# Kernel optimization log

Measured on AMD Instinct MI355X. Metric: run time of the kernel, lower is better.

Reference implementation:

```python
import jax, jax.numpy as jnp
import numpy as np

GROUPS = 8
EPS = 1e-5


def group_norm(x, gamma, beta):
    b, c, h, w = x.shape
    xg = x.reshape(b, GROUPS, c // GROUPS, h, w)
    mu = jnp.mean(xg, axis=(2, 3, 4), keepdims=True)
    var = jnp.mean((xg - mu) ** 2, axis=(2, 3, 4), keepdims=True)
    xn = ((xg - mu) * jax.lax.rsqrt(var + EPS)).reshape(b, c, h, w)
    return xn * gamma[None, :, None, None] + beta[None, :, None, None]


def setup_inputs() -> dict:
    key = jax.random.key(0)
    ks = jax.random.split(key, 4)
    b, c, h, w = 4, 64, 64, 64
    x = jax.random.normal(ks[0], (b, c, h, w), dtype=jnp.float32)
    gamma = jnp.ones((c,), dtype=jnp.float32)
    beta = jnp.zeros((c,), dtype=jnp.float32)
    w_qkv = jax.random.normal(ks[1], (3 * c, c), dtype=jnp.float32) * (1.0 / np.sqrt(c))
    b_qkv = jnp.zeros((3 * c,), dtype=jnp.float32)
    w_proj = jax.random.normal(ks[2], (c, c), dtype=jnp.float32) * (1.0 / np.sqrt(c))
    b_proj = jnp.zeros((c,), dtype=jnp.float32)
    return {"x": x, "gamma": gamma, "beta": beta, "w_qkv": w_qkv,
            "b_qkv": b_qkv, "w_proj": w_proj, "b_proj": b_proj}


def reference(x, gamma, beta, w_qkv, b_qkv, w_proj, b_proj):
    b, c, h, w = x.shape
    xn = group_norm(x, gamma, beta)
    # 1x1 conv == per-pixel linear: [b,3c,h,w]
    qkv = jnp.einsum('oc,bchw->bohw', w_qkv, xn) + b_qkv[None, :, None, None]
    q, k, v = jnp.split(qkv, 3, axis=1)
    # flatten spatial -> tokens: [b, hw, c]
    def tok(t):
        return t.reshape(b, c, h * w).transpose(0, 2, 1)
    q, k, v = tok(q), tok(k), tok(v)
    scale = c ** (-0.5)
    attn = jnp.einsum('bqc,bkc->bqk', q, k) * scale  # [b, hw, hw]
    attn = jax.nn.softmax(attn, axis=-1)
    out = jnp.einsum('bqk,bkc->bqc', attn, v)  # [b, hw, c]
    out = out.transpose(0, 2, 1).reshape(b, c, h, w)
    out = jnp.einsum('oc,bchw->bohw', w_proj, out) + b_proj[None, :, None, None]
    return out + x
```

## Files before the change

kernel.cpp:

```cpp
#include <hip/hip_runtime.h>

typedef __bf16 bf16x8 __attribute__((ext_vector_type(8)));
typedef __bf16 bf16x4 __attribute__((ext_vector_type(4)));
typedef float  f32x4  __attribute__((ext_vector_type(4)));
typedef float  f32x16 __attribute__((ext_vector_type(16)));

#define GLD_LDS16(gsrc, ldst) \
  __builtin_amdgcn_global_load_lds((const __attribute__((address_space(1))) void*)(gsrc), \
                                   (__attribute__((address_space(3))) void*)(ldst), 16, 0, 0)

__device__ inline unsigned cvt_pk_bf16(float lo, float hi) {
  unsigned r;
  asm("v_cvt_pk_bf16_f32 %0, %1, %2" : "=v"(r) : "v"(lo), "v"(hi));
  return r;
}
__device__ inline void pl32_swap(unsigned& a, unsigned& b) {
  asm volatile("v_permlane32_swap_b32 %0, %1" : "+v"(a), "+v"(b));
}
__device__ inline f32x16 zero16() {
  f32x16 z;
#pragma unroll
  for (int i = 0; i < 16; ++i) z[i] = 0.f;
  return z;
}

__global__ __launch_bounds__(256) void gn_partial_k(const float* __restrict__ x,
                                                    const float* __restrict__ w_qkv,
                                                    float* __restrict__ partial,
                                                    __bf16* __restrict__ whi,
                                                    __bf16* __restrict__ wlo) {
  __shared__ float red[2][4];
  const int t = threadIdx.x;
  if (blockIdx.x < 48) {
    const int idx = blockIdx.x * 256 + t;
    float wv = w_qkv[idx];
    __bf16 hh = (__bf16)wv;
    whi[idx] = hh;
    wlo[idx] = (__bf16)(wv - (float)hh);
  }
  const float4* base = (const float4*)(x + (size_t)blockIdx.x * 4096);
  float s = 0.f, sq = 0.f;
#pragma unroll
  for (int kk = 0; kk < 4; ++kk) {
    float4 v = base[t + kk * 256];
    s  += (v.x + v.y) + (v.z + v.w);
    sq += (v.x * v.x + v.y * v.y) + (v.z * v.z + v.w * v.w);
  }
#pragma unroll
  for (int o = 32; o >= 1; o >>= 1) {
    s  += __shfl_down(s, o, 64);
    sq += __shfl_down(sq, o, 64);
  }
  if ((t & 63) == 0) { red[0][t >> 6] = s; red[1][t >> 6] = sq; }
  __syncthreads();
  if (t == 0) {
    float S  = (red[0][0] + red[0][1]) + (red[0][2] + red[0][3]);
    float SQ = (red[1][0] + red[1][1]) + (red[1][2] + red[1][3]);
    partial[blockIdx.x * 2]     = S;
    partial[blockIdx.x * 2 + 1] = SQ;
  }
}

__global__ void gn_final_k(const float* __restrict__ partial,
                           const float* __restrict__ gamma,
                           const float* __restrict__ beta,
                           float* __restrict__ sc) {
  const int t = threadIdx.x;
  __shared__ float mu_s[32], rs_s[32];
  if (t < 32) {
    float S = 0.f, SQ = 0.f;
#pragma unroll
    for (int i = 0; i < 8; ++i) {
      S  += partial[(t * 8 + i) * 2];
      SQ += partial[(t * 8 + i) * 2 + 1];
    }
    float mean = S * (1.f / 32768.f);
    float var  = SQ * (1.f / 32768.f) - mean * mean;
    mu_s[t] = mean;
    rs_s[t] = rsqrtf(fmaxf(var, 0.f) + 1e-5f);
  }
  __syncthreads();
  const int b = t >> 6, c = t & 63;
  const int g = b * 8 + (c >> 3);
  float scale = rs_s[g] * gamma[c];
  sc[t * 2]     = scale;
  sc[t * 2 + 1] = beta[c] - mu_s[g] * scale;
}

__global__ __launch_bounds__(256) void qkv_k(const float* __restrict__ x,
                                             const float* __restrict__ sc,
                                             const __bf16* __restrict__ whi,
                                             const __bf16* __restrict__ wlo,
                                             const float* __restrict__ b_qkv,
                                             __bf16* __restrict__ qo,
                                             __bf16* __restrict__ ko,
                                             __bf16* __restrict__ vto) {
  const int tid  = threadIdx.x;
  const int lane = tid & 63, w = tid >> 6;
  const int px16 = lane & 15, grp = lane >> 4;
  const int b    = blockIdx.x >> 6;
  const int s0   = (blockIdx.x & 63) * 64;
  const int pxg  = s0 + w * 16 + px16;

  bf16x8 bh[2], bl[2];
#pragma unroll
  for (int kk = 0; kk < 2; ++kk) {
    bf16x8 hv, lv;
#pragma unroll
    for (int i = 0; i < 8; ++i) {
      const int c = kk * 32 + grp * 8 + i;
      float xv = x[((size_t)(b * 64 + c) * 4096) + pxg];
      float2 s = *(const float2*)(sc + (b * 64 + c) * 2);
      float xn = fmaf(xv, s.x, s.y);
      __bf16 hh = (__bf16)xn;
      hv[i] = hh;
      lv[i] = (__bf16)(xn - (float)hh);
    }
    bh[kk] = hv;
    bl[kk] = lv;
  }

  f32x4 acc[12];
#pragma unroll
  for (int ot = 0; ot < 12; ++ot) {
    const int o = ot * 16 + px16;
    f32x4 a = {0.f, 0.f, 0.f, 0.f};
#pragma unroll
    for (int kk = 0; kk < 2; ++kk) {
      const size_t wo = (size_t)o * 64 + kk * 32 + grp * 8;
      bf16x8 ah = *(const bf16x8*)(whi + wo);
      bf16x8 al = *(const bf16x8*)(wlo + wo);
      a = __builtin_amdgcn_mfma_f32_16x16x32_bf16(ah, bh[kk], a, 0, 0, 0);
      a = __builtin_amdgcn_mfma_f32_16x16x32_bf16(ah, bl[kk], a, 0, 0, 0);
      a = __builtin_amdgcn_mfma_f32_16x16x32_bf16(al, bh[kk], a, 0, 0, 0);
    }
    acc[ot] = a;
  }

#pragma unroll
  for (int ot = 0; ot < 4; ++ot) {
    const int ob = ot * 16 + grp * 4;
    float4 bias = *(const float4*)(b_qkv + ob);
    f32x4 a = acc[ot];
    bf16x4 qv = {(__bf16)((a[0] + bias.x) * 0.18033688f),
                 (__bf16)((a[1] + bias.y) * 0.18033688f),
                 (__bf16)((a[2] + bias.z) * 0.18033688f),
                 (__bf16)((a[3] + bias.w) * 0.18033688f)};
    *(bf16x4*)(qo + ((size_t)b * 4096 + pxg) * 64 + ob) = qv;
  }
#pragma unroll
  for (int ot = 4; ot < 8; ++ot) {
    const int ob = (ot - 4) * 16 + grp * 4;
    float4 bias = *(const float4*)(b_qkv + 64 + ob);
    f32x4 a = acc[ot];
    bf16x4 kv = {(__bf16)(a[0] + bias.x), (__bf16)(a[1] + bias.y),
                 (__bf16)(a[2] + bias.z), (__bf16)(a[3] + bias.w)};
    *(bf16x4*)(ko + ((size_t)b * 4096 + pxg) * 64 + ob) = kv;
  }
#pragma unroll
  for (int ot = 8; ot < 12; ++ot) {
    const int ob = (ot - 8) * 16 + grp * 4;
    float4 bias = *(const float4*)(b_qkv + 128 + ob);
    f32x4 a = acc[ot];
#pragma unroll
    for (int r = 0; r < 4; ++r) {
      float bv = (r == 0) ? bias.x : (r == 1) ? bias.y : (r == 2) ? bias.z : bias.w;
      vto[((size_t)(b * 64 + ob + r)) * 4096 + pxg] = (__bf16)(a[r] + bv);
    }
  }
}

__global__ __launch_bounds__(512, 2) void attn_k(const __bf16* __restrict__ q,
                                                 const __bf16* __restrict__ k,
                                                 const __bf16* __restrict__ vt,
                                                 __bf16* __restrict__ opart,
                                                 float* __restrict__ mlpart) {
  __shared__ __bf16 k_lds[3][4096];
  __shared__ __bf16 v_lds[3][4096];

  const int tid  = threadIdx.x;
  const int lane = tid & 63, w = tid >> 6;
  const int col  = lane & 31;
  const int h    = lane >> 5;
  const int swz  = col & 7;

  const int blk  = blockIdx.x;
  const int xcd  = blk & 7;
  const int b    = xcd >> 1;
  const int rest = blk >> 3;
  const int seg  = rest >> 3;
  const int qblk = (rest & 7) | ((xcd & 1) << 3);
  const int q0   = qblk * 256 + w * 32;
  const int j0b  = seg * 512;

  const __bf16* qp = q  + (size_t)b * 4096 * 64;
  const __bf16* kp = k  + (size_t)b * 4096 * 64;
  const __bf16* vp = vt + (size_t)b * 64 * 4096;

  bf16x8 qf[4];
#pragma unroll
  for (int kk = 0; kk < 4; ++kk)
    qf[kk] = *(const bf16x8*)(qp + (size_t)(q0 + col) * 64 + kk * 16 + h * 8);
  __builtin_amdgcn_sched_barrier(0);

  f32x16 acc0 = zero16(), acc1 = zero16();
  float m = -1e30f, l = 0.f;

  const int soff = tid * 16;
  const int sj = soff >> 7;
  const int sc2 = ((soff >> 4) & 7) ^ (sj & 7);

  auto stage = [&](int buf, int j0) {
    GLD_LDS16(kp + (size_t)(j0 + sj) * 64 + sc2 * 8, (char*)(&k_lds[buf][0]) + soff);
    GLD_LDS16(vp + (size_t)sj * 4096 + j0 + sc2 * 8, (char*)(&v_lds[buf][0]) + soff);
  };

  stage(0, j0b);
  stage(1, j0b + 64);

#pragma unroll
  for (int kt = 0; kt < 8; ++kt) {
    if (kt < 7) asm volatile("s_waitcnt vmcnt(2)" ::: "memory");
    else        asm volatile("s_waitcnt vmcnt(0)" ::: "memory");
    __builtin_amdgcn_s_barrier();

    if (kt < 6) stage((kt + 2) % 3, j0b + (kt + 2) * 64);

    const char* kbase = (const char*)&k_lds[kt % 3][0];
    const char* vbase = (const char*)&v_lds[kt % 3][0];

    f32x16 sa0 = zero16(), sa1 = zero16();
    __builtin_amdgcn_s_setprio(1);
#pragma unroll
    for (int kk = 0; kk < 4; ++kk) {
      bf16x8 kf0 = *(const bf16x8*)(kbase + col * 128        + (((2 * kk + h) ^ swz) << 4));
      bf16x8 kf1 = *(const bf16x8*)(kbase + (32 + col) * 128 + (((2 * kk + h) ^ swz) << 4));
      sa0 = __builtin_amdgcn_mfma_f32_32x32x16_bf16(kf0, qf[kk], sa0, 0, 0, 0);
      sa1 = __builtin_amdgcn_mfma_f32_32x32x16_bf16(kf1, qf[kk], sa1, 0, 0, 0);
    }
    __builtin_amdgcn_s_setprio(0);

    float x0 = fmaxf(fmaxf(sa0[0], sa0[1]),   fmaxf(sa0[2], sa0[3]));
    float x1 = fmaxf(fmaxf(sa0[4], sa0[5]),   fmaxf(sa0[6], sa0[7]));
    float x2 = fmaxf(fmaxf(sa0[8], sa0[9]),   fmaxf(sa0[10], sa0[11]));
    float x3 = fmaxf(fmaxf(sa0[12], sa0[13]), fmaxf(sa0[14], sa0[15]));
    float y0 = fmaxf(fmaxf(sa1[0], sa1[1]),   fmaxf(sa1[2], sa1[3]));
    float y1 = fmaxf(fmaxf(sa1[4], sa1[5]),   fmaxf(sa1[6], sa1[7]));
    float y2 = fmaxf(fmaxf(sa1[8], sa1[9]),   fmaxf(sa1[10], sa1[11]));
    float y3 = fmaxf(fmaxf(sa1[12], sa1[13]), fmaxf(sa1[14], sa1[15]));
    float mx = fmaxf(fmaxf(fmaxf(x0, x1), fmaxf(x2, x3)),
                     fmaxf(fmaxf(y0, y1), fmaxf(y2, y3)));
    mx = fmaxf(mx, __shfl_xor(mx, 32, 64));
    float mn = fmaxf(m, mx);
    float sf = exp2f(m - mn);
    m = mn;
    float ls = 0.f;
#pragma unroll
    for (int r = 0; r < 16; ++r) { sa0[r] = exp2f(sa0[r] - mn); ls += sa0[r]; }
#pragma unroll
    for (int r = 0; r < 16; ++r) { sa1[r] = exp2f(sa1[r] - mn); ls += sa1[r]; }
    l = l * sf + ls;
    acc0 *= sf;
    acc1 *= sf;

    unsigned w0[8], w1[8];
#pragma unroll
    for (int qd = 0; qd < 4; ++qd) {
      w0[qd * 2]     = cvt_pk_bf16(sa0[4 * qd],     sa0[4 * qd + 1]);
      w0[qd * 2 + 1] = cvt_pk_bf16(sa0[4 * qd + 2], sa0[4 * qd + 3]);
      w1[qd * 2]     = cvt_pk_bf16(sa1[4 * qd],     sa1[4 * qd + 1]);
      w1[qd * 2 + 1] = cvt_pk_bf16(sa1[4 * qd + 2], sa1[4 * qd + 3]);
    }
    bf16x8 pa[4];
#pragma unroll
    for (int c = 0; c < 4; ++c) {
      const unsigned* wt = (c < 2) ? w0 : w1;
      unsigned a0 = wt[(2 * (c & 1)) * 2],     b0 = wt[(2 * (c & 1) + 1) * 2];
      unsigned a1 = wt[(2 * (c & 1)) * 2 + 1], b1 = wt[(2 * (c & 1) + 1) * 2 + 1];
      pl32_swap(a0, b0);
      pl32_swap(a1, b1);
      uint4 u; u.x = a0; u.y = a1; u.z = b0; u.w = b1;
      pa[c] = __builtin_bit_cast(bf16x8, u);
    }

    __builtin_amdgcn_s_setprio(1);
#pragma unroll
    for (int c = 0; c < 4; ++c) {
      bf16x8 vf0 = *(const bf16x8*)(vbase + col * 128        + (((2 * c + h) ^ swz) << 4));
      bf16x8 vf1 = *(const bf16x8*)(vbase + (32 + col) * 128 + (((2 * c + h) ^ swz) << 4));
      acc0 = __builtin_amdgcn_mfma_f32_32x32x16_bf16(vf0, pa[c], acc0, 0, 0, 0);
      acc1 = __builtin_amdgcn_mfma_f32_32x32x16_bf16(vf1, pa[c], acc1, 0, 0, 0);
    }
    __builtin_amdgcn_s_setprio(0);
  }

  float lf = l + __shfl_xor(l, 32, 64);
  const int qrow = q0 + col;
  __bf16* ob = opart + ((size_t)(b * 8 + seg) * 4096 + qrow) * 64;
#pragma unroll
  for (int rq = 0; rq < 4; ++rq) {
    const int d0 = 8 * rq + 4 * h;
    bf16x4 o0 = {(__bf16)acc0[4 * rq], (__bf16)acc0[4 * rq + 1],
                 (__bf16)acc0[4 * rq + 2], (__bf16)acc0[4 * rq + 3]};
    bf16x4 o1 = {(__bf16)acc1[4 * rq], (__bf16)acc1[4 * rq + 1],
                 (__bf16)acc1[4 * rq + 2], (__bf16)acc1[4 * rq + 3]};
    *(bf16x4*)(ob + d0)      = o0;
    *(bf16x4*)(ob + 32 + d0) = o1;
  }
  if (h == 0) {
    float2 mlv; mlv.x = m; mlv.y = lf;
    *(float2*)(mlpart + ((size_t)(b * 8 + seg) * 4096 + qrow) * 2) = mlv;
  }
}

__global__ __launch_bounds__(256) void proj_k(const __bf16* __restrict__ opart,
                                              const float* __restrict__ mlpart,
                                              const float* __restrict__ x,
                                              const float* __restrict__ w_proj,
                                              const float* __restrict__ b_proj,
                                              float* __restrict__ out) {
  __shared__ float wseg[8][32];
  __shared__ float a_lds[32 * 68];
  __shared__ float o_lds[64 * 33];
  const int t  = threadIdx.x;
  const int b  = blockIdx.x >> 7;
  const int s0 = (blockIdx.x & 127) * 32;

  if (t < 32) {
    const int rowg = s0 + t;
    float ms[8], ls[8], es[8];
    float M = -1e30f;
#pragma unroll
    for (int s = 0; s < 8; ++s) {
      float2 ml = *(const float2*)(mlpart + ((size_t)(b * 8 + s) * 4096 + rowg) * 2);
      ms[s] = ml.x; ls[s] = ml.y;
      M = fmaxf(M, ms[s]);
    }
    float L = 0.f;
#pragma unroll
    for (int s = 0; s < 8; ++s) { es[s] = exp2f(ms[s] - M); L += es[s] * ls[s]; }
    float invL = 1.f / L;
#pragma unroll
    for (int s = 0; s < 8; ++s) wseg[s][t] = es[s] * invL;
  }
  __syncthreads();

  for (int i = t; i < 512; i += 256) {
    const int px = i >> 4, c4 = i & 15;
    const __bf16* obase = opart + ((size_t)(b * 8) * 4096 + s0 + px) * 64 + c4 * 4;
    float4 a = {0.f, 0.f, 0.f, 0.f};
#pragma unroll
    for (int s = 0; s < 8; ++s) {
      bf16x4 v = *(const bf16x4*)(obase + (size_t)s * 4096 * 64);
      float wv = wseg[s][px];
      a.x += wv * (float)v[0]; a.y += wv * (float)v[1];
      a.z += wv * (float)v[2]; a.w += wv * (float)v[3];
    }
    *(float4*)(&a_lds[px * 68 + c4 * 4]) = a;
  }

  const int o = t & 63, wg = t >> 6;
  float4 wr[16];
  const float4* wrow = (const float4*)(w_proj + o * 64);
#pragma unroll
  for (int i = 0; i < 16; ++i) wr[i] = wrow[i];
  const float bias = b_proj[o];
  __syncthreads();

  for (int pp = 0; pp < 8; ++pp) {
    const int px = wg * 8 + pp;
    const float4* ar = (const float4*)&a_lds[px * 68];
    float a0 = bias, a1 = 0.f, a2 = 0.f, a3 = 0.f;
#pragma unroll
    for (int i = 0; i < 16; i += 4) {
      float4 x0 = ar[i], x1 = ar[i + 1], x2 = ar[i + 2], x3 = ar[i + 3];
      a0 += wr[i    ].x * x0.x + wr[i    ].y * x0.y + wr[i    ].z * x0.z + wr[i    ].w * x0.w;
      a1 += wr[i + 1].x * x1.x + wr[i + 1].y * x1.y + wr[i + 1].z * x1.z + wr[i + 1].w * x1.w;
      a2 += wr[i + 2].x * x2.x + wr[i + 2].y * x2.y + wr[i + 2].z * x2.z + wr[i + 2].w * x2.w;
      a3 += wr[i + 3].x * x3.x + wr[i + 3].y * x3.y + wr[i + 3].z * x3.z + wr[i + 3].w * x3.w;
    }
    o_lds[o * 33 + px] = (a0 + a1) + (a2 + a3);
  }
  __syncthreads();
  for (int idx = t; idx < 2048; idx += 256) {
    const int c = idx >> 5, px = idx & 31;
    const size_t gi = ((size_t)(b * 64 + c)) * 4096 + s0 + px;
    out[gi] = o_lds[c * 33 + px] + x[gi];
  }
}

extern "C" void kernel_launch(void* const* d_in, const int* in_sizes, int n_in,
                              void* d_out, int out_size, void* d_ws, size_t ws_size,
                              hipStream_t stream) {
  const float* x      = (const float*)d_in[0];
  const float* gamma  = (const float*)d_in[1];
  const float* beta   = (const float*)d_in[2];
  const float* w_qkv  = (const float*)d_in[3];
  const float* b_qkv  = (const float*)d_in[4];
  const float* w_proj = (const float*)d_in[5];
  const float* b_proj = (const float*)d_in[6];
  float* out = (float*)d_out;

  char* ws = (char*)d_ws;
  float*  partial = (float*)ws;
  float*  scbuf   = partial + 512;
  __bf16* whi     = (__bf16*)(ws + 4096);
  __bf16* wlo     = whi + 12288;
  __bf16* qb  = (__bf16*)(ws + 65536);
  __bf16* kb  = qb  + (size_t)4 * 4096 * 64;
  __bf16* vtb = kb  + (size_t)4 * 4096 * 64;
  __bf16* opart = vtb + (size_t)4 * 4096 * 64;
  float*  mlpart = (float*)(opart + (size_t)4 * 8 * 4096 * 64);

  gn_partial_k<<<256, 256, 0, stream>>>(x, w_qkv, partial, whi, wlo);
  gn_final_k<<<1, 256, 0, stream>>>(partial, gamma, beta, scbuf);
  qkv_k<<<256, 256, 0, stream>>>(x, scbuf, whi, wlo, b_qkv, qb, kb, vtb);
  attn_k<<<512, 512, 0, stream>>>(qb, kb, vtb, opart, mlpart);
  proj_k<<<512, 256, 0, stream>>>(opart, mlpart, x, w_proj, b_proj, out);
}
```

Before: 71.53 us.

## Fuse group-norm finalize into QKV and restructure attention staging with lazy rescale

Removes the single-block gn_final kernel by having each qkv block compute its batch's group statistics and per-channel scale/shift into shared memory, eliminating one launch and a global round trip. The attention kernel switches from a 3-deep per-tile ring to four LDS buffers loaded two tiles at a time with fewer barriers. It also skips the online-softmax rescale of the accumulators when the new row max exceeds the running max by at most 8. This raises LDS use per block and shortens prefetch depth between waits, trading overlap for fewer synchronisations and fewer rescales.

```diff
diff --git a/kernel.cpp b/kernel.cpp
--- a/kernel.cpp
+++ b/kernel.cpp
@@ -61,40 +61,17 @@
   }
 }
 
-__global__ void gn_final_k(const float* __restrict__ partial,
-                           const float* __restrict__ gamma,
-                           const float* __restrict__ beta,
-                           float* __restrict__ sc) {
-  const int t = threadIdx.x;
-  __shared__ float mu_s[32], rs_s[32];
-  if (t < 32) {
-    float S = 0.f, SQ = 0.f;
-#pragma unroll
-    for (int i = 0; i < 8; ++i) {
-      S  += partial[(t * 8 + i) * 2];
-      SQ += partial[(t * 8 + i) * 2 + 1];
-    }
-    float mean = S * (1.f / 32768.f);
-    float var  = SQ * (1.f / 32768.f) - mean * mean;
-    mu_s[t] = mean;
-    rs_s[t] = rsqrtf(fmaxf(var, 0.f) + 1e-5f);
-  }
-  __syncthreads();
-  const int b = t >> 6, c = t & 63;
-  const int g = b * 8 + (c >> 3);
-  float scale = rs_s[g] * gamma[c];
-  sc[t * 2]     = scale;
-  sc[t * 2 + 1] = beta[c] - mu_s[g] * scale;
-}
-
 __global__ __launch_bounds__(256) void qkv_k(const float* __restrict__ x,
-                                             const float* __restrict__ sc,
+                                             const float* __restrict__ partial,
+                                             const float* __restrict__ gamma,
+                                             const float* __restrict__ beta,
                                              const __bf16* __restrict__ whi,
                                              const __bf16* __restrict__ wlo,
                                              const float* __restrict__ b_qkv,
                                              __bf16* __restrict__ qo,
                                              __bf16* __restrict__ ko,
                                              __bf16* __restrict__ vto) {
+  __shared__ float mu_s[8], rs_s[8], sc_l[128];
   const int tid  = threadIdx.x;
   const int lane = tid & 63, w = tid >> 6;
   const int px16 = lane & 15, grp = lane >> 4;
@@ -102,6 +79,27 @@
   const int s0   = (blockIdx.x & 63) * 64;
   const int pxg  = s0 + w * 16 + px16;
 
+  if (tid < 8) {
+    float S = 0.f, SQ = 0.f;
+#pragma unroll
+    for (int i = 0; i < 8; ++i) {
+      S  += partial[((b * 8 + tid) * 8 + i) * 2];
+      SQ += partial[((b * 8 + tid) * 8 + i) * 2 + 1];
+    }
+    float mean = S * (1.f / 32768.f);
+    float var  = SQ * (1.f / 32768.f) - mean * mean;
+    mu_s[tid] = mean;
+    rs_s[tid] = rsqrtf(fmaxf(var, 0.f) + 1e-5f);
+  }
+  __syncthreads();
+  if (tid < 64) {
+    const int g = tid >> 3;
+    float scale = rs_s[g] * gamma[tid];
+    sc_l[tid * 2]     = scale;
+    sc_l[tid * 2 + 1] = beta[tid] - mu_s[g] * scale;
+  }
+  __syncthreads();
+
   bf16x8 bh[2], bl[2];
 #pragma unroll
   for (int kk = 0; kk < 2; ++kk) {
@@ -110,8 +108,7 @@
     for (int i = 0; i < 8; ++i) {
       const int c = kk * 32 + grp * 8 + i;
       float xv = x[((size_t)(b * 64 + c) * 4096) + pxg];
-      float2 s = *(const float2*)(sc + (b * 64 + c) * 2);
-      float xn = fmaf(xv, s.x, s.y);
+      float xn = fmaf(xv, sc_l[c * 2], sc_l[c * 2 + 1]);
       __bf16 hh = (__bf16)xn;
       hv[i] = hh;
       lv[i] = (__bf16)(xn - (float)hh);
@@ -175,8 +172,8 @@
                                                  const __bf16* __restrict__ vt,
                                                  __bf16* __restrict__ opart,
                                                  float* __restrict__ mlpart) {
-  __shared__ __bf16 k_lds[3][4096];
-  __shared__ __bf16 v_lds[3][4096];
+  __shared__ __bf16 k_lds[4][4096];
+  __shared__ __bf16 v_lds[4][4096];
 
   const int tid  = threadIdx.x;
   const int lane = tid & 63, w = tid >> 6;
@@ -217,81 +214,91 @@
 
   stage(0, j0b);
   stage(1, j0b + 64);
-
-#pragma unroll
-  for (int kt = 0; kt < 8; ++kt) {
-    if (kt < 7) asm volatile("s_waitcnt vmcnt(2)" ::: "memory");
-    else        asm volatile("s_waitcnt vmcnt(0)" ::: "memory");
+  stage(2, j0b + 128);
+  stage(3, j0b + 192);
+
+#pragma unroll
+  for (int kt = 0; kt < 4; ++kt) {
+    if (kt == 0) asm volatile("s_waitcnt vmcnt(4)" ::: "memory");
+    else         asm volatile("s_waitcnt vmcnt(0)" ::: "memory");
     __builtin_amdgcn_s_barrier();
 
-    if (kt < 6) stage((kt + 2) % 3, j0b + (kt + 2) * 64);
-
-    const char* kbase = (const char*)&k_lds[kt % 3][0];
-    const char* vbase = (const char*)&v_lds[kt % 3][0];
-
-    f32x16 sa0 = zero16(), sa1 = zero16();
-    __builtin_amdgcn_s_setprio(1);
-#pragma unroll
-    for (int kk = 0; kk < 4; ++kk) {
-      bf16x8 kf0 = *(const bf16x8*)(kbase + col * 128        + (((2 * kk + h) ^ swz) << 4));
-      bf16x8 kf1 = *(const bf16x8*)(kbase + (32 + col) * 128 + (((2 * kk + h) ^ swz) << 4));
-      sa0 = __builtin_amdgcn_mfma_f32_32x32x16_bf16(kf0, qf[kk], sa0, 0, 0, 0);
-      sa1 = __builtin_amdgcn_mfma_f32_32x32x16_bf16(kf1, qf[kk], sa1, 0, 0, 0);
-    }
-    __builtin_amdgcn_s_setprio(0);
-
-    float x0 = fmaxf(fmaxf(sa0[0], sa0[1]),   fmaxf(sa0[2], sa0[3]));
-    float x1 = fmaxf(fmaxf(sa0[4], sa0[5]),   fmaxf(sa0[6], sa0[7]));
-    float x2 = fmaxf(fmaxf(sa0[8], sa0[9]),   fmaxf(sa0[10], sa0[11]));
-    float x3 = fmaxf(fmaxf(sa0[12], sa0[13]), fmaxf(sa0[14], sa0[15]));
-    float y0 = fmaxf(fmaxf(sa1[0], sa1[1]),   fmaxf(sa1[2], sa1[3]));
-    float y1 = fmaxf(fmaxf(sa1[4], sa1[5]),   fmaxf(sa1[6], sa1[7]));
-    float y2 = fmaxf(fmaxf(sa1[8], sa1[9]),   fmaxf(sa1[10], sa1[11]));
-    float y3 = fmaxf(fmaxf(sa1[12], sa1[13]), fmaxf(sa1[14], sa1[15]));
-    float mx = fmaxf(fmaxf(fmaxf(x0, x1), fmaxf(x2, x3)),
-                     fmaxf(fmaxf(y0, y1), fmaxf(y2, y3)));
-    mx = fmaxf(mx, __shfl_xor(mx, 32, 64));
-    float mn = fmaxf(m, mx);
-    float sf = exp2f(m - mn);
-    m = mn;
-    float ls = 0.f;
-#pragma unroll
-    for (int r = 0; r < 16; ++r) { sa0[r] = exp2f(sa0[r] - mn); ls += sa0[r]; }
-#pragma unroll
-    for (int r = 0; r < 16; ++r) { sa1[r] = exp2f(sa1[r] - mn); ls += sa1[r]; }
-    l = l * sf + ls;
-    acc0 *= sf;
-    acc1 *= sf;
-
-    unsigned w0[8], w1[8];
-#pragma unroll
-    for (int qd = 0; qd < 4; ++qd) {
-      w0[qd * 2]     = cvt_pk_bf16(sa0[4 * qd],     sa0[4 * qd + 1]);
-      w0[qd * 2 + 1] = cvt_pk_bf16(sa0[4 * qd + 2], sa0[4 * qd + 3]);
-      w1[qd * 2]     = cvt_pk_bf16(sa1[4 * qd],     sa1[4 * qd + 1]);
-      w1[qd * 2 + 1] = cvt_pk_bf16(sa1[4 * qd + 2], sa1[4 * qd + 3]);
-    }
-    bf16x8 pa[4];
-#pragma unroll
-    for (int c = 0; c < 4; ++c) {
-      const unsigned* wt = (c < 2) ? w0 : w1;
-      unsigned a0 = wt[(2 * (c & 1)) * 2],     b0 = wt[(2 * (c & 1) + 1) * 2];
-      unsigned a1 = wt[(2 * (c & 1)) * 2 + 1], b1 = wt[(2 * (c & 1) + 1) * 2 + 1];
-      pl32_swap(a0, b0);
-      pl32_swap(a1, b1);
-      uint4 u; u.x = a0; u.y = a1; u.z = b0; u.w = b1;
-      pa[c] = __builtin_bit_cast(bf16x8, u);
-    }
-
-    __builtin_amdgcn_s_setprio(1);
-#pragma unroll
-    for (int c = 0; c < 4; ++c) {
-      bf16x8 vf0 = *(const bf16x8*)(vbase + col * 128        + (((2 * c + h) ^ swz) << 4));
-      bf16x8 vf1 = *(const bf16x8*)(vbase + (32 + col) * 128 + (((2 * c + h) ^ swz) << 4));
-      acc0 = __builtin_amdgcn_mfma_f32_32x32x16_bf16(vf0, pa[c], acc0, 0, 0, 0);
-      acc1 = __builtin_amdgcn_mfma_f32_32x32x16_bf16(vf1, pa[c], acc1, 0, 0, 0);
-    }
-    __builtin_amdgcn_s_setprio(0);
+    if (kt == 1) { stage(0, j0b + 256); stage(1, j0b + 320); }
+    if (kt == 2) { stage(2, j0b + 384); stage(3, j0b + 448); }
+
+#pragma unroll
+    for (int sub = 0; sub < 2; ++sub) {
+      const int buf = (2 * kt + sub) & 3;
+      const char* kbase = (const char*)&k_lds[buf][0];
+      const char* vbase = (const char*)&v_lds[buf][0];
+
+      f32x16 sa0 = zero16(), sa1 = zero16();
+      __builtin_amdgcn_s_setprio(1);
+#pragma unroll
+      for (int kk = 0; kk < 4; ++kk) {
+        bf16x8 kf0 = *(const bf16x8*)(kbase + col * 128        + (((2 * kk + h) ^ swz) << 4));
+        bf16x8 kf1 = *(const bf16x8*)(kbase + (32 + col) * 128 + (((2 * kk + h) ^ swz) << 4));
+        sa0 = __builtin_amdgcn_mfma_f32_32x32x16_bf16(kf0, qf[kk], sa0, 0, 0, 0);
+        sa1 = __builtin_amdgcn_mfma_f32_32x32x16_bf16(kf1, qf[kk], sa1, 0, 0, 0);
+      }
+      __builtin_amdgcn_s_setprio(0);
+
+      float x0 = fmaxf(fmaxf(sa0[0], sa0[1]),   fmaxf(sa0[2], sa0[3]));
+      float x1 = fmaxf(fmaxf(sa0[4], sa0[5]),   fmaxf(sa0[6], sa0[7]));
+      float x2 = fmaxf(fmaxf(sa0[8], sa0[9]),   fmaxf(sa0[10], sa0[11]));
+      float x3 = fmaxf(fmaxf(sa0[12], sa0[13]), fmaxf(sa0[14], sa0[15]));
+      float y0 = fmaxf(fmaxf(sa1[0], sa1[1]),   fmaxf(sa1[2], sa1[3]));
+      float y1 = fmaxf(fmaxf(sa1[4], sa1[5]),   fmaxf(sa1[6], sa1[7]));
+      float y2 = fmaxf(fmaxf(sa1[8], sa1[9]),   fmaxf(sa1[10], sa1[11]));
+      float y3 = fmaxf(fmaxf(sa1[12], sa1[13]), fmaxf(sa1[14], sa1[15]));
+      float mx = fmaxf(fmaxf(fmaxf(x0, x1), fmaxf(x2, x3)),
+                       fmaxf(fmaxf(y0, y1), fmaxf(y2, y3)));
+      mx = fmaxf(mx, __shfl_xor(mx, 32, 64));
+      if (!__all(mx <= m + 8.f)) {
+        float mn = fmaxf(m, mx);
+        float sf = exp2f(m - mn);
+        m = mn;
+        l *= sf;
+        acc0 *= sf;
+        acc1 *= sf;
+      }
+      float ls = 0.f;
+#pragma unroll
+      for (int r = 0; r < 16; ++r) { sa0[r] = exp2f(sa0[r] - m); ls += sa0[r]; }
+#pragma unroll
+      for (int r = 0; r < 16; ++r) { sa1[r] = exp2f(sa1[r] - m); ls += sa1[r]; }
+      l += ls;
+
+      unsigned w0[8], w1[8];
+#pragma unroll
+      for (int qd = 0; qd < 4; ++qd) {
+        w0[qd * 2]     = cvt_pk_bf16(sa0[4 * qd],     sa0[4 * qd + 1]);
+        w0[qd * 2 + 1] = cvt_pk_bf16(sa0[4 * qd + 2], sa0[4 * qd + 3]);
+        w1[qd * 2]     = cvt_pk_bf16(sa1[4 * qd],     sa1[4 * qd + 1]);
+        w1[qd * 2 + 1] = cvt_pk_bf16(sa1[4 * qd + 2], sa1[4 * qd + 3]);
+      }
+      bf16x8 pa[4];
+#pragma unroll
+      for (int c = 0; c < 4; ++c) {
+        const unsigned* wt = (c < 2) ? w0 : w1;
+        unsigned a0 = wt[(2 * (c & 1)) * 2],     b0 = wt[(2 * (c & 1) + 1) * 2];
+        unsigned a1 = wt[(2 * (c & 1)) * 2 + 1], b1 = wt[(2 * (c & 1) + 1) * 2 + 1];
+        pl32_swap(a0, b0);
+        pl32_swap(a1, b1);
+        uint4 u; u.x = a0; u.y = a1; u.z = b0; u.w = b1;
+        pa[c] = __builtin_bit_cast(bf16x8, u);
+      }
+
+      __builtin_amdgcn_s_setprio(1);
+#pragma unroll
+      for (int c = 0; c < 4; ++c) {
+        bf16x8 vf0 = *(const bf16x8*)(vbase + col * 128        + (((2 * c + h) ^ swz) << 4));
+        bf16x8 vf1 = *(const bf16x8*)(vbase + (32 + col) * 128 + (((2 * c + h) ^ swz) << 4));
+        acc0 = __builtin_amdgcn_mfma_f32_32x32x16_bf16(vf0, pa[c], acc0, 0, 0, 0);
+        acc1 = __builtin_amdgcn_mfma_f32_32x32x16_bf16(vf1, pa[c], acc1, 0, 0, 0);
+      }
+      __builtin_amdgcn_s_setprio(0);
+    }
   }
 
   float lf = l + __shfl_xor(l, 32, 64);
@@ -403,7 +410,6 @@
 
   char* ws = (char*)d_ws;
   float*  partial = (float*)ws;
-  float*  scbuf   = partial + 512;
   __bf16* whi     = (__bf16*)(ws + 4096);
   __bf16* wlo     = whi + 12288;
   __bf16* qb  = (__bf16*)(ws + 65536);
@@ -413,8 +419,7 @@
   float*  mlpart = (float*)(opart + (size_t)4 * 8 * 4096 * 64);
 
   gn_partial_k<<<256, 256, 0, stream>>>(x, w_qkv, partial, whi, wlo);
-  gn_final_k<<<1, 256, 0, stream>>>(partial, gamma, beta, scbuf);
-  qkv_k<<<256, 256, 0, stream>>>(x, scbuf, whi, wlo, b_qkv, qb, kb, vtb);
+  qkv_k<<<256, 256, 0, stream>>>(x, partial, gamma, beta, whi, wlo, b_qkv, qb, kb, vtb);
   attn_k<<<512, 512, 0, stream>>>(qb, kb, vtb, opart, mlpart);
   proj_k<<<512, 256, 0, stream>>>(opart, mlpart, x, w_proj, b_proj, out);
 }
```

New measurement: 67.81 us, median of 2. -5.2%, faster.
